# Performance work log

Measured on AMD Instinct MI355X. Metric: run time of the kernel, lower is better.

Reference implementation:

```python
import jax, jax.numpy as jnp
import numpy as np

TOP_K = 2
EPS = 1e-10


def setup_inputs() -> dict:
    key = jax.random.key(0)
    k1, k2 = jax.random.split(key)
    B, S, D, E = 4, 4096, 4096, 64
    hidden_states = jax.random.normal(k1, (B, S, D), dtype=jnp.float32)
    # router weight, scaled like a standard linear init
    w_router = jax.random.normal(k2, (D, E), dtype=jnp.float32) / np.sqrt(D)
    return {"hidden_states": hidden_states, "w_router": w_router}


def reference(hidden_states, w_router):
    # router: [B,S,D] x [D,E] -> [B,S,E]
    router_logits = jnp.einsum("bsd,de->bse", hidden_states, w_router)
    # balanced_assignment: softmax, global load, penalty, adjusted top-k
    routing_probs = jax.nn.softmax(router_logits, axis=-1)
    current_load = routing_probs.sum(axis=(0, 1))            # [E]
    load_penalty = current_load / (current_load.mean() + EPS)  # [E]
    adjusted_logits = router_logits - jnp.log(load_penalty + EPS)
    _, expert_indices = jax.lax.top_k(adjusted_logits, TOP_K)  # [B,S,top_k]
    return adjusted_logits, expert_indices
```

## Files before the change

kernel.cpp:

```cpp
#include <hip/hip_runtime.h>
#include <math.h>

#define ROWS 16384
#define DD   4096
#define EE   64
#define EPSF 1e-10f

#define BM    32
#define KT    64
#define NKT   (DD / KT)
#define WTILE 12288
#define BTILE (2 * WTILE)

typedef __attribute__((ext_vector_type(8))) short short8;
typedef __attribute__((ext_vector_type(4))) float f32x4;
typedef __attribute__((ext_vector_type(4))) unsigned u32x4;

__device__ __forceinline__ void split3x8(const float f[8], u32x4& w0,
                                         u32x4& w1, u32x4& w2) {
#pragma unroll
  for (int i = 0; i < 4; ++i) {
    float fa = f[2 * i], fb = f[2 * i + 1];
    unsigned ua = __float_as_uint(fa), ub = __float_as_uint(fb);
    unsigned ra = ua + 0x7fffu + ((ua >> 16) & 1u);
    unsigned rb = ub + 0x7fffu + ((ub >> 16) & 1u);
    w0[i] = (rb & 0xffff0000u) | (ra >> 16);
    fa -= __uint_as_float(ra & 0xffff0000u);
    fb -= __uint_as_float(rb & 0xffff0000u);
    ua = __float_as_uint(fa); ub = __float_as_uint(fb);
    ra = ua + 0x7fffu + ((ua >> 16) & 1u);
    rb = ub + 0x7fffu + ((ub >> 16) & 1u);
    w1[i] = (rb & 0xffff0000u) | (ra >> 16);
    fa -= __uint_as_float(ra & 0xffff0000u);
    fb -= __uint_as_float(rb & 0xffff0000u);
    ua = __float_as_uint(fa); ub = __float_as_uint(fb);
    ra = ua + 0x7fffu + ((ua >> 16) & 1u);
    rb = ub + 0x7fffu + ((ub >> 16) & 1u);
    w2[i] = (rb & 0xffff0000u) | (ra >> 16);
  }
}

__device__ __forceinline__ void dma16(const void* g, void* l) {
  __builtin_amdgcn_global_load_lds(
      (const __attribute__((address_space(1))) unsigned int*)g,
      (__attribute__((address_space(3))) unsigned int*)l, 16, 0, 0);
}

__global__ __launch_bounds__(256) void k_wsplit(const float* __restrict__ wr,
                                                unsigned char* __restrict__ out,
                                                float* __restrict__ g_load) {
  const int kt = blockIdx.x;
  const int t = threadIdx.x;
  const int lane = t & 63, wv = t >> 6;
  if (blockIdx.x == 0 && t < 64) g_load[t] = 0.f;
  float f[8];
  const float* wp = wr + (size_t)(kt * 32 + wv * 8) * EE + lane;
#pragma unroll
  for (int j = 0; j < 8; ++j) f[j] = wp[(size_t)j * EE];
  u32x4 w0, w1, w2;
  split3x8(f, w0, w1, w2);
  const int et = lane >> 4;
  const int lp = wv * 16 + (lane & 15);
  unsigned char* base = out + (size_t)kt * WTILE + et * 1024 + lp * 16;
  *(u32x4*)(base + 0 * 4096) = w0;
  *(u32x4*)(base + 1 * 4096) = w1;
  *(u32x4*)(base + 2 * 4096) = w2;
}

__global__ __launch_bounds__(256) void k_gemm(
    const float* __restrict__ h, const unsigned char* __restrict__ wsp,
    float* __restrict__ logits, float* __restrict__ g_load) {
  __shared__ alignas(16) unsigned char smem[2 * BTILE];

  const int t = threadIdx.x;
  const int lane = t & 63;
  const int wv = t >> 6;
  const int mt = wv >> 1;
  const int eh = wv & 1;
  const int row0 = blockIdx.x * BM;

  f32x4 acc[2] = {};

  const float* ap =
      h + (size_t)(row0 + mt * 16 + (lane & 15)) * DD + (lane >> 4) * 8;
  const int dmaoff = t * 16;

  float4 c0, c1, c2, c3, n0, n1, n2, n3;

#pragma unroll
  for (int i = 0; i < 6; ++i)
    dma16(wsp + i * 4096 + dmaoff, smem + i * 4096 + dmaoff);
  c0 = *(const float4*)(ap);
  c1 = *(const float4*)(ap + 4);
  c2 = *(const float4*)(ap + 32);
  c3 = *(const float4*)(ap + 36);

  for (int kt = 0; kt < NKT; ++kt) {
    const int buf = kt & 1;
    asm volatile("s_waitcnt vmcnt(0)" ::: "memory");
    __syncthreads();

    if (kt + 1 < NKT) {
      const unsigned char* ws = wsp + (size_t)(kt + 1) * BTILE;
      unsigned char* nb = smem + (buf ^ 1) * BTILE;
#pragma unroll
      for (int i = 0; i < 6; ++i)
        dma16(ws + i * 4096 + dmaoff, nb + i * 4096 + dmaoff);
      const float* p = ap + (size_t)(kt + 1) * KT;
      n0 = *(const float4*)(p);
      n1 = *(const float4*)(p + 4);
      n2 = *(const float4*)(p + 32);
      n3 = *(const float4*)(p + 36);
    }

    const unsigned char* lb = smem + buf * BTILE;
#pragma unroll
    for (int sub = 0; sub < 2; ++sub) {
      const unsigned char* sb = lb + sub * WTILE;
      short8 bf[3][2];
#pragma unroll
      for (int p = 0; p < 3; ++p)
#pragma unroll
        for (int e = 0; e < 2; ++e)
          bf[p][e] =
              *(const short8*)&sb[p * 4096 + (eh * 2 + e) * 1024 + lane * 16];

      const float4 a0 = sub ? c2 : c0;
      const float4 a1 = sub ? c3 : c1;
      const float af[8] = {a0.x, a0.y, a0.z, a0.w, a1.x, a1.y, a1.z, a1.w};
      u32x4 q0, q1, q2;
      split3x8(af, q0, q1, q2);
      const short8 ah0 = __builtin_bit_cast(short8, q0);
      const short8 ah1 = __builtin_bit_cast(short8, q1);
      const short8 ah2 = __builtin_bit_cast(short8, q2);
#pragma unroll
      for (int e = 0; e < 2; ++e) {
        f32x4 c = acc[e];
        c = __builtin_amdgcn_mfma_f32_16x16x32_bf16(ah0, bf[0][e], c, 0, 0, 0);
        c = __builtin_amdgcn_mfma_f32_16x16x32_bf16(ah0, bf[1][e], c, 0, 0, 0);
        c = __builtin_amdgcn_mfma_f32_16x16x32_bf16(ah1, bf[0][e], c, 0, 0, 0);
        c = __builtin_amdgcn_mfma_f32_16x16x32_bf16(ah0, bf[2][e], c, 0, 0, 0);
        c = __builtin_amdgcn_mfma_f32_16x16x32_bf16(ah1, bf[1][e], c, 0, 0, 0);
        c = __builtin_amdgcn_mfma_f32_16x16x32_bf16(ah2, bf[0][e], c, 0, 0, 0);
        acc[e] = c;
      }
    }

    if (kt + 1 < NKT) { c0 = n0; c1 = n1; c2 = n2; c3 = n3; }
  }

  asm volatile("s_waitcnt vmcnt(0)" ::: "memory");
  __syncthreads();
  float* sl = (float*)smem;
  {
    const int rb = mt * 16 + (lane >> 4) * 4;
    const int cb = eh * 32 + (lane & 15);
#pragma unroll
    for (int e = 0; e < 2; ++e)
#pragma unroll
      for (int r = 0; r < 4; ++r)
        sl[(rb + r) * 68 + cb + e * 16] = acc[e][r];
  }
  __syncthreads();

  float accp = 0.f;
#pragma unroll
  for (int i = 0; i < 8; ++i) {
    const int row = wv * 8 + i;
    const float x = sl[row * 68 + lane];
    float m = x;
#pragma unroll
    for (int off = 32; off > 0; off >>= 1) m = fmaxf(m, __shfl_xor(m, off, 64));
    const float p = __expf(x - m);
    float s = p;
#pragma unroll
    for (int off = 32; off > 0; off >>= 1) s += __shfl_xor(s, off, 64);
    accp += p / s;
    logits[(size_t)(row0 + row) * EE + lane] = x;
  }
  float* red = sl + 32 * 68;
  red[wv * 64 + lane] = accp;
  __syncthreads();
  if (wv == 0) {
    float s = red[0 * 64 + lane] + red[1 * 64 + lane] + red[2 * 64 + lane] +
              red[3 * 64 + lane];
    atomicAdd(&g_load[lane], s);
  }
}

__global__ __launch_bounds__(256) void k_top2(float* __restrict__ logits,
                                              const float* __restrict__ g_load,
                                              float* __restrict__ idx_out) {
  int t = threadIdx.x;
  int lane = t & 63;
  int wv = t >> 6;
  int row = blockIdx.x * 4 + wv;

  float v0 = g_load[lane];
  float s0 = v0;
#pragma unroll
  for (int off = 32; off > 0; off >>= 1) s0 += __shfl_xor(s0, off, 64);
  float lp = logf(v0 / (s0 * (1.f / 64.f) + EPSF) + EPSF);

  size_t base = (size_t)row * EE;
  float a = logits[base + lane] - lp;
  logits[base + lane] = a;

  float v = a;
  int idx = lane;
#pragma unroll
  for (int off = 32; off > 0; off >>= 1) {
    float ov = __shfl_xor(v, off, 64);
    int oi = __shfl_xor(idx, off, 64);
    if (ov > v || (ov == v && oi < idx)) { v = ov; idx = oi; }
  }
  int i1 = idx;

  float a2 = (lane == i1) ? -INFINITY : a;
  v = a2;
  idx = lane;
#pragma unroll
  for (int off = 32; off > 0; off >>= 1) {
    float ov = __shfl_xor(v, off, 64);
    int oi = __shfl_xor(idx, off, 64);
    if (ov > v || (ov == v && oi < idx)) { v = ov; idx = oi; }
  }
  int i2 = idx;

  if (lane == 0) {
    idx_out[(size_t)row * 2 + 0] = (float)i1;
    idx_out[(size_t)row * 2 + 1] = (float)i2;
  }
}

extern "C" void kernel_launch(void* const* d_in, const int* in_sizes, int n_in,
                              void* d_out, int out_size, void* d_ws,
                              size_t ws_size, hipStream_t stream) {
  const float* h = (const float*)d_in[0];
  const float* wr = (const float*)d_in[1];
  float* out = (float*)d_out;
  float* logits = out;
  float* idx_out = out + (size_t)ROWS * EE;
  float* g_load = (float*)d_ws;
  unsigned char* wsp = (unsigned char*)d_ws + 512;

  k_wsplit<<<DD / 32, 256, 0, stream>>>(wr, wsp, g_load);
  k_gemm<<<ROWS / BM, 256, 0, stream>>>(h, wsp, logits, g_load);
  k_top2<<<ROWS / 4, 256, 0, stream>>>(logits, g_load, idx_out);
}
```

Baseline: 426.4 us.

## Double GEMM row tile to 64 with 512 threads and split-K across wave pairs

Each gemm block now covers 64 rows with 8 waves. Each wave pair splits the K tile in half, and each wave computes all 64 experts for its 16 rows. The two K halves are summed through shared memory before the softmax and load reduction. The aim is to halve how often the shared weight tile is loaded per row and to cut the number of blocks. The cost is more accumulator registers, an extra reduction pass, and fewer, larger blocks.

```diff
diff --git a/kernel.cpp b/kernel.cpp
--- a/kernel.cpp
+++ b/kernel.cpp
@@ -6,7 +6,7 @@
 #define EE   64
 #define EPSF 1e-10f
 
-#define BM    32
+#define BM    64
 #define KT    64
 #define NKT   (DD / KT)
 #define WTILE 12288
@@ -67,7 +67,7 @@
   *(u32x4*)(base + 2 * 4096) = w2;
 }
 
-__global__ __launch_bounds__(256) void k_gemm(
+__global__ __launch_bounds__(512) void k_gemm(
     const float* __restrict__ h, const unsigned char* __restrict__ wsp,
     float* __restrict__ logits, float* __restrict__ g_load) {
   __shared__ alignas(16) unsigned char smem[2 * BTILE];
@@ -76,24 +76,22 @@
   const int lane = t & 63;
   const int wv = t >> 6;
   const int mt = wv >> 1;
-  const int eh = wv & 1;
+  const int sub = wv & 1;
   const int row0 = blockIdx.x * BM;
 
-  f32x4 acc[2] = {};
-
-  const float* ap =
-      h + (size_t)(row0 + mt * 16 + (lane & 15)) * DD + (lane >> 4) * 8;
+  f32x4 acc[4] = {};
+
+  const float* ap = h + (size_t)(row0 + mt * 16 + (lane & 15)) * DD +
+                    sub * 32 + (lane >> 4) * 8;
   const int dmaoff = t * 16;
 
-  float4 c0, c1, c2, c3, n0, n1, n2, n3;
-
-#pragma unroll
-  for (int i = 0; i < 6; ++i)
-    dma16(wsp + i * 4096 + dmaoff, smem + i * 4096 + dmaoff);
+  float4 c0, c1, n0, n1;
+
+#pragma unroll
+  for (int i = 0; i < 3; ++i)
+    dma16(wsp + i * 8192 + dmaoff, smem + i * 8192 + dmaoff);
   c0 = *(const float4*)(ap);
   c1 = *(const float4*)(ap + 4);
-  c2 = *(const float4*)(ap + 32);
-  c3 = *(const float4*)(ap + 36);
 
   for (int kt = 0; kt < NKT; ++kt) {
     const int buf = kt & 1;
@@ -104,49 +102,40 @@
       const unsigned char* ws = wsp + (size_t)(kt + 1) * BTILE;
       unsigned char* nb = smem + (buf ^ 1) * BTILE;
 #pragma unroll
-      for (int i = 0; i < 6; ++i)
-        dma16(ws + i * 4096 + dmaoff, nb + i * 4096 + dmaoff);
+      for (int i = 0; i < 3; ++i)
+        dma16(ws + i * 8192 + dmaoff, nb + i * 8192 + dmaoff);
       const float* p = ap + (size_t)(kt + 1) * KT;
       n0 = *(const float4*)(p);
       n1 = *(const float4*)(p + 4);
-      n2 = *(const float4*)(p + 32);
-      n3 = *(const float4*)(p + 36);
-    }
-
-    const unsigned char* lb = smem + buf * BTILE;
-#pragma unroll
-    for (int sub = 0; sub < 2; ++sub) {
-      const unsigned char* sb = lb + sub * WTILE;
-      short8 bf[3][2];
-#pragma unroll
-      for (int p = 0; p < 3; ++p)
-#pragma unroll
-        for (int e = 0; e < 2; ++e)
-          bf[p][e] =
-              *(const short8*)&sb[p * 4096 + (eh * 2 + e) * 1024 + lane * 16];
-
-      const float4 a0 = sub ? c2 : c0;
-      const float4 a1 = sub ? c3 : c1;
-      const float af[8] = {a0.x, a0.y, a0.z, a0.w, a1.x, a1.y, a1.z, a1.w};
-      u32x4 q0, q1, q2;
-      split3x8(af, q0, q1, q2);
-      const short8 ah0 = __builtin_bit_cast(short8, q0);
-      const short8 ah1 = __builtin_bit_cast(short8, q1);
-      const short8 ah2 = __builtin_bit_cast(short8, q2);
-#pragma unroll
-      for (int e = 0; e < 2; ++e) {
-        f32x4 c = acc[e];
-        c = __builtin_amdgcn_mfma_f32_16x16x32_bf16(ah0, bf[0][e], c, 0, 0, 0);
-        c = __builtin_amdgcn_mfma_f32_16x16x32_bf16(ah0, bf[1][e], c, 0, 0, 0);
-        c = __builtin_amdgcn_mfma_f32_16x16x32_bf16(ah1, bf[0][e], c, 0, 0, 0);
-        c = __builtin_amdgcn_mfma_f32_16x16x32_bf16(ah0, bf[2][e], c, 0, 0, 0);
-        c = __builtin_amdgcn_mfma_f32_16x16x32_bf16(ah1, bf[1][e], c, 0, 0, 0);
-        c = __builtin_amdgcn_mfma_f32_16x16x32_bf16(ah2, bf[0][e], c, 0, 0, 0);
-        acc[e] = c;
-      }
-    }
-
-    if (kt + 1 < NKT) { c0 = n0; c1 = n1; c2 = n2; c3 = n3; }
+    }
+
+    const unsigned char* lb = smem + buf * BTILE + sub * WTILE;
+    short8 bf[3][4];
+#pragma unroll
+    for (int p = 0; p < 3; ++p)
+#pragma unroll
+      for (int e = 0; e < 4; ++e)
+        bf[p][e] = *(const short8*)&lb[p * 4096 + e * 1024 + lane * 16];
+
+    const float af[8] = {c0.x, c0.y, c0.z, c0.w, c1.x, c1.y, c1.z, c1.w};
+    u32x4 q0, q1, q2;
+    split3x8(af, q0, q1, q2);
+    const short8 ah0 = __builtin_bit_cast(short8, q0);
+    const short8 ah1 = __builtin_bit_cast(short8, q1);
+    const short8 ah2 = __builtin_bit_cast(short8, q2);
+#pragma unroll
+    for (int e = 0; e < 4; ++e) {
+      f32x4 c = acc[e];
+      c = __builtin_amdgcn_mfma_f32_16x16x32_bf16(ah0, bf[0][e], c, 0, 0, 0);
+      c = __builtin_amdgcn_mfma_f32_16x16x32_bf16(ah0, bf[1][e], c, 0, 0, 0);
+      c = __builtin_amdgcn_mfma_f32_16x16x32_bf16(ah1, bf[0][e], c, 0, 0, 0);
+      c = __builtin_amdgcn_mfma_f32_16x16x32_bf16(ah0, bf[2][e], c, 0, 0, 0);
+      c = __builtin_amdgcn_mfma_f32_16x16x32_bf16(ah1, bf[1][e], c, 0, 0, 0);
+      c = __builtin_amdgcn_mfma_f32_16x16x32_bf16(ah2, bf[0][e], c, 0, 0, 0);
+      acc[e] = c;
+    }
+
+    if (kt + 1 < NKT) { c0 = n0; c1 = n1; }
   }
 
   asm volatile("s_waitcnt vmcnt(0)" ::: "memory");
@@ -154,14 +143,24 @@
   float* sl = (float*)smem;
   {
     const int rb = mt * 16 + (lane >> 4) * 4;
-    const int cb = eh * 32 + (lane & 15);
-#pragma unroll
-    for (int e = 0; e < 2; ++e)
-#pragma unroll
-      for (int r = 0; r < 4; ++r)
-        sl[(rb + r) * 68 + cb + e * 16] = acc[e][r];
-  }
-  __syncthreads();
+    const int cb = lane & 15;
+    if (sub == 0) {
+#pragma unroll
+      for (int e = 0; e < 4; ++e)
+#pragma unroll
+        for (int r = 0; r < 4; ++r)
+          sl[(rb + r) * 68 + e * 16 + cb] = acc[e][r];
+    }
+    __syncthreads();
+    if (sub == 1) {
+#pragma unroll
+      for (int e = 0; e < 4; ++e)
+#pragma unroll
+        for (int r = 0; r < 4; ++r)
+          sl[(rb + r) * 68 + e * 16 + cb] += acc[e][r];
+    }
+    __syncthreads();
+  }
 
   float accp = 0.f;
 #pragma unroll
@@ -178,12 +177,13 @@
     accp += p / s;
     logits[(size_t)(row0 + row) * EE + lane] = x;
   }
-  float* red = sl + 32 * 68;
+  float* red = sl + 64 * 68;
   red[wv * 64 + lane] = accp;
   __syncthreads();
   if (wv == 0) {
-    float s = red[0 * 64 + lane] + red[1 * 64 + lane] + red[2 * 64 + lane] +
-              red[3 * 64 + lane];
+    float s = 0.f;
+#pragma unroll
+    for (int j = 0; j < 8; ++j) s += red[j * 64 + lane];
     atomicAdd(&g_load[lane], s);
   }
 }
@@ -245,6 +245,6 @@
   unsigned char* wsp = (unsigned char*)d_ws + 512;
 
   k_wsplit<<<DD / 32, 256, 0, stream>>>(wr, wsp, g_load);
-  k_gemm<<<ROWS / BM, 256, 0, stream>>>(h, wsp, logits, g_load);
+  k_gemm<<<ROWS / BM, 512, 0, stream>>>(h, wsp, logits, g_load);
   k_top2<<<ROWS / 4, 256, 0, stream>>>(logits, g_load, idx_out);
 }
```

New measurement: 408.0 us. 4.3% less time.
